# Performance work log

Measured on AMD Instinct MI355X. Metric: run time of the kernel, lower is better.

Reference implementation:

```python
import jax, jax.numpy as jnp
import numpy as np
import math

D_MODEL = 1024
N_HEADS = 16
D_K = D_MODEL // N_HEADS
B, S = 2, 2048


def setup_inputs() -> dict:
    key = jax.random.key(0)
    ks = jax.random.split(key, 11)
    sc = 1.0 / math.sqrt(D_MODEL)
    inp = {
        'q': jax.random.normal(ks[0], (B, S, D_MODEL), jnp.float32),
        'k': jax.random.normal(ks[1], (B, S, D_MODEL), jnp.float32),
        'v': jax.random.normal(ks[2], (B, S, D_MODEL), jnp.float32),
        'mask': jnp.tril(jnp.ones((S, S), jnp.int32))[None, None],  # [1,1,S,S] causal
        'W_q': jax.random.normal(ks[3], (D_MODEL, D_MODEL), jnp.float32) * sc,
        'b_q': jnp.zeros((D_MODEL,), jnp.float32),
        'W_k': jax.random.normal(ks[4], (D_MODEL, D_MODEL), jnp.float32) * sc,
        'b_k': jnp.zeros((D_MODEL,), jnp.float32),
        'W_v': jax.random.normal(ks[5], (D_MODEL, D_MODEL), jnp.float32) * sc,
        'b_v': jnp.zeros((D_MODEL,), jnp.float32),
        'W_o': jax.random.normal(ks[6], (D_MODEL, D_MODEL), jnp.float32) * sc,
        'b_o': jnp.zeros((D_MODEL,), jnp.float32),
    }
    return inp


def reference(q, k, v, mask, W_q, b_q, W_k, b_k, W_v, b_v, W_o, b_o):
    # Linear projections then split heads: [B,S,D] -> [B,H,S,d_k]
    def split_heads(x):
        b, s, _ = x.shape
        return x.reshape(b, s, N_HEADS, D_K).transpose(0, 2, 1, 3)

    Q = split_heads(q @ W_q + b_q)
    K = split_heads(k @ W_k + b_k)
    V = split_heads(v @ W_v + b_v)

    scores = jnp.einsum('bhqd,bhkd->bhqk', Q, K) / math.sqrt(D_K)
    scores = jnp.where(mask == 0, jnp.float32(-1e9), scores)
    attn = jax.nn.softmax(scores, axis=-1)  # dropout is identity in eval mode
    out = jnp.einsum('bhqk,bhkd->bhqd', attn, V)
    out = out.transpose(0, 2, 1, 3).reshape(q.shape[0], -1, D_MODEL)
    return out @ W_o + b_o
```

## Files before the change

kernel.cpp:

```cpp
#include <hip/hip_runtime.h>
#include <hip/hip_bf16.h>

#define D_MODEL 1024
#define S_LEN   2048
#define BATCH   2
#define NH      16
#define DK      64

typedef __bf16 bf16_t;
typedef __attribute__((ext_vector_type(8))) __bf16 bf16x8;
typedef __attribute__((ext_vector_type(4))) float f32x4;

#if __has_builtin(__builtin_amdgcn_exp2f)
#define EXP2F(x) __builtin_amdgcn_exp2f(x)
#else
#define EXP2F(x) exp2f(x)
#endif

#define Q_SCALE 0.1803368801111204f

#define GLDS16(gp, lp) __builtin_amdgcn_global_load_lds( \
    (const __attribute__((address_space(1))) void*)(gp), \
    (__attribute__((address_space(3))) void*)(lp), 16, 0, 0)

__global__ __launch_bounds__(256) void prep(
    const float* __restrict__ q, const float* __restrict__ k, const float* __restrict__ v,
    const float* __restrict__ Wq, const float* __restrict__ Wk,
    const float* __restrict__ Wv, const float* __restrict__ Wo,
    bf16_t* __restrict__ qkvb, bf16_t* __restrict__ WqkvT, bf16_t* __restrict__ WoT)
{
    __shared__ float t[32][33];
    const int tid = threadIdx.x;
    if (blockIdx.z < 3) {
        const long NELEM = (long)BATCH * S_LEN * D_MODEL;
        const float* src = (blockIdx.z == 0) ? q : (blockIdx.z == 1) ? k : v;
        long i = ((long)blockIdx.x * 256 + tid) * 8;
        float4 a = *(const float4*)(src + i);
        float4 b = *(const float4*)(src + i + 4);
        bf16x8 o;
        o[0] = (bf16_t)a.x; o[1] = (bf16_t)a.y; o[2] = (bf16_t)a.z; o[3] = (bf16_t)a.w;
        o[4] = (bf16_t)b.x; o[5] = (bf16_t)b.y; o[6] = (bf16_t)b.z; o[7] = (bf16_t)b.w;
        *(bf16x8*)(qkvb + blockIdx.z * NELEM + i) = o;
    } else {
        int wz = (blockIdx.z - 3) * 2048 + blockIdx.x;
        int mat = wz >> 10;
        int tile = wz & 1023;
        int bx = tile & 31, by = tile >> 5;
        const float* in = (mat == 0) ? Wq : (mat == 1) ? Wk : (mat == 2) ? Wv : Wo;
        bf16_t* out = (mat < 3) ? (WqkvT + (long)mat * D_MODEL * D_MODEL) : WoT;
        int tx = tid & 31, ty = tid >> 5;
        int gx = bx * 32, gy = by * 32;
#pragma unroll
        for (int i = 0; i < 32; i += 8)
            t[ty + i][tx] = in[(gy + ty + i) * D_MODEL + gx + tx];
        __syncthreads();
#pragma unroll
        for (int i = 0; i < 32; i += 8)
            out[(gx + ty + i) * D_MODEL + gy + tx] = (bf16_t)t[tx][ty + i];
    }
}

#define BM 128
#define BN 128
#define BKT 64

__device__ __forceinline__ void swizzle_xy(int bx, int by, int& n0, int& m0) {
    int lin = by * 8 + bx;
    n0 = (lin >> 5) * BN;
    m0 = (lin & 31) * BM;
}

template <int ROWS>
__device__ __forceinline__ void stage_swz(const bf16_t* __restrict__ G, int row0,
                                          int k0, bf16_t* __restrict__ Ls, int tid) {
#pragma unroll
    for (int it = 0; it < ROWS / 32; ++it) {
        int g = it * 256 + tid;
        int row = g >> 3;
        int c = (g & 7) ^ (row & 7);
        GLDS16(&G[(long)(row0 + row) * D_MODEL + k0 + c * 8],
               &Ls[(it * 256 + (tid & ~63)) * 8]);
    }
}

__device__ __forceinline__ bf16x8 frag_swz(const bf16_t* __restrict__ Ls, int row, int cg) {
    return *(const bf16x8*)(&Ls[(row * 8 + (cg ^ (row & 7))) * 8]);
}

constexpr int QKV_SMEM = (BM * BKT + BN * BKT) > (128 * 136) ? (BM * BKT + BN * BKT)
                                                             : (128 * 136);
__global__ __launch_bounds__(256) void gemm_qkv(
    const bf16_t* __restrict__ qkvb, const bf16_t* __restrict__ WqkvT,
    const float* __restrict__ bq, const float* __restrict__ bk, const float* __restrict__ bv,
    bf16_t* __restrict__ Qw, bf16_t* __restrict__ Kw, bf16_t* __restrict__ Vt)
{
    __shared__ __align__(16) bf16_t smem[QKV_SMEM];
    bf16_t* As = smem;
    bf16_t* Bs = smem + BM * BKT;
    const int z = blockIdx.z;
    const bf16_t* A  = qkvb + (long)z * BATCH * S_LEN * D_MODEL;
    const bf16_t* BT = WqkvT + (long)z * D_MODEL * D_MODEL;
    const float* bias = (z == 0) ? bq : (z == 1) ? bk : bv;
    bf16_t* Cb = (z == 0) ? Qw : (z == 1) ? Kw : Vt;
    const float oscale = (z == 0) ? Q_SCALE : 1.0f;

    const int tid  = threadIdx.x;
    const int wave = tid >> 6, lane = tid & 63;
    const int lrow = lane & 15, kgrp = lane >> 4;
    const int wm = (wave >> 1) * 64, wn = (wave & 1) * 64;
    int m0, n0;
    swizzle_xy(blockIdx.x, blockIdx.y, n0, m0);

    f32x4 acc[4][4] = {};

    for (int k0 = 0; k0 < D_MODEL; k0 += BKT) {
        stage_swz<BM>(A, m0, k0, As, tid);
        stage_swz<BN>(BT, n0, k0, Bs, tid);
        __syncthreads();
#pragma unroll
        for (int kk = 0; kk < 2; ++kk) {
            bf16x8 af[4], bfr[4];
#pragma unroll
            for (int mi = 0; mi < 4; ++mi)
                af[mi] = frag_swz(As, wm + mi * 16 + lrow, kk * 4 + kgrp);
#pragma unroll
            for (int ni = 0; ni < 4; ++ni)
                bfr[ni] = frag_swz(Bs, wn + ni * 16 + lrow, kk * 4 + kgrp);
#pragma unroll
            for (int mi = 0; mi < 4; ++mi)
#pragma unroll
                for (int ni = 0; ni < 4; ++ni)
                    acc[mi][ni] = __builtin_amdgcn_mfma_f32_16x16x32_bf16(af[mi], bfr[ni], acc[mi][ni], 0, 0, 0);
        }
        __syncthreads();
    }

    if (z != 2) {
#pragma unroll
        for (int mi = 0; mi < 4; ++mi)
#pragma unroll
            for (int ni = 0; ni < 4; ++ni) {
                int col = n0 + wn + ni * 16 + lrow;
                float bvf = bias[col];
#pragma unroll
                for (int r = 0; r < 4; ++r) {
                    int row = m0 + wm + mi * 16 + kgrp * 4 + r;
                    float vv = (acc[mi][ni][r] + bvf) * oscale;
                    int b = row >> 11, s = row & (S_LEN - 1);
                    int h = col >> 6, d = col & (DK - 1);
                    Cb[(((long)(b * NH + h) * S_LEN + s) * DK) + d] = (bf16_t)vv;
                }
            }
    } else {
        bf16_t* Ct = smem;
#pragma unroll
        for (int mi = 0; mi < 4; ++mi)
#pragma unroll
            for (int ni = 0; ni < 4; ++ni) {
                int cl = wn + ni * 16 + lrow;
                float bvf = bias[n0 + cl];
#pragma unroll
                for (int r = 0; r < 4; ++r) {
                    int rl = wm + mi * 16 + kgrp * 4 + r;
                    Ct[cl * 136 + rl] = (bf16_t)(acc[mi][ni][r] + bvf);
                }
            }
        __syncthreads();
        const int b = m0 >> 11, sbase = m0 & (S_LEN - 1);
#pragma unroll
        for (int pass = 0; pass < 4; ++pass) {
            int dl = pass * 32 + (tid >> 3);
            int sc = (tid & 7) * 16;
            int colg = n0 + dl;
            int h = colg >> 6, d = colg & (DK - 1);
            bf16_t* dst = Cb + (((long)(b * NH + h) * DK + d) * S_LEN + sbase + sc);
            *(bf16x8*)(dst)     = *(const bf16x8*)&Ct[dl * 136 + sc];
            *(bf16x8*)(dst + 8) = *(const bf16x8*)&Ct[dl * 136 + sc + 8];
        }
    }
}

#define OM 64
__global__ __launch_bounds__(256) void gemm_out(
    const bf16_t* __restrict__ A, const bf16_t* __restrict__ BT,
    const float* __restrict__ bias, float* __restrict__ Cf)
{
    __shared__ __align__(16) bf16_t As[OM * BKT];
    __shared__ __align__(16) bf16_t Bs[BN * BKT];
    const int tid  = threadIdx.x;
    const int wave = tid >> 6, lane = tid & 63;
    const int lrow = lane & 15, kgrp = lane >> 4;
    const int wm = (wave >> 1) * 32, wn = (wave & 1) * 64;
    int lin = blockIdx.y * 8 + blockIdx.x;
    int m0 = (lin & 63) * OM;
    int n0 = (lin >> 6) * BN;

    f32x4 acc[2][4] = {};

    for (int k0 = 0; k0 < D_MODEL; k0 += BKT) {
        stage_swz<OM>(A, m0, k0, As, tid);
        stage_swz<BN>(BT, n0, k0, Bs, tid);
        __syncthreads();
#pragma unroll
        for (int kk = 0; kk < 2; ++kk) {
            bf16x8 af[2], bfr[4];
#pragma unroll
            for (int mi = 0; mi < 2; ++mi)
                af[mi] = frag_swz(As, wm + mi * 16 + lrow, kk * 4 + kgrp);
#pragma unroll
            for (int ni = 0; ni < 4; ++ni)
                bfr[ni] = frag_swz(Bs, wn + ni * 16 + lrow, kk * 4 + kgrp);
#pragma unroll
            for (int mi = 0; mi < 2; ++mi)
#pragma unroll
                for (int ni = 0; ni < 4; ++ni)
                    acc[mi][ni] = __builtin_amdgcn_mfma_f32_16x16x32_bf16(af[mi], bfr[ni], acc[mi][ni], 0, 0, 0);
        }
        __syncthreads();
    }

#pragma unroll
    for (int mi = 0; mi < 2; ++mi)
#pragma unroll
        for (int ni = 0; ni < 4; ++ni) {
            int col = n0 + wn + ni * 16 + lrow;
            float bvf = bias[col];
#pragma unroll
            for (int r = 0; r < 4; ++r) {
                int row = m0 + wm + mi * 16 + kgrp * 4 + r;
                Cf[(long)row * D_MODEL + col] = acc[mi][ni][r] + bvf;
            }
        }
}

__device__ __forceinline__ void attn_one_qtile(
    int qi, int bh, int wave, int lrow, int kgrp,
    int r0, int c0, int r1,
    const bf16_t* __restrict__ Qh, const bf16_t* __restrict__ Kh,
    const bf16_t* __restrict__ Vth, bf16_t* __restrict__ O,
    bf16_t* __restrict__ Ks, bf16_t* __restrict__ Vs, bf16_t* __restrict__ Pw)
{
    const int q0 = qi * 64;
    const int qrow = q0 + wave * 16;

    bf16x8 qf[2];
#pragma unroll
    for (int kk = 0; kk < 2; ++kk)
        qf[kk] = *(const bf16x8*)(&Qh[(qrow + lrow) * DK + kk * 32 + kgrp * 8]);

    f32x4 acc[4] = {};
    float lsum[4] = {0.f, 0.f, 0.f, 0.f};

    const int nt = qi + 1;

    uint4 kpre0 = *(const uint4*)(&Kh[(long)r0 * DK + c0]);
    uint4 kpre1 = *(const uint4*)(&Kh[(long)r1 * DK + c0]);
    uint4 vpre0 = *(const uint4*)(&Vth[(long)r0 * S_LEN + c0]);
    uint4 vpre1 = *(const uint4*)(&Vth[(long)r1 * S_LEN + c0]);

    for (int t = 0; t < nt; ++t) {
        __syncthreads();
        *(uint4*)(&Ks[r0 * 72 + c0]) = kpre0;
        *(uint4*)(&Ks[r1 * 72 + c0]) = kpre1;
        *(uint4*)(&Vs[r0 * 72 + c0]) = vpre0;
        *(uint4*)(&Vs[r1 * 72 + c0]) = vpre1;
        if (t + 1 < nt) {
            const int j0n = (t + 1) * 64;
            kpre0 = *(const uint4*)(&Kh[(long)(j0n + r0) * DK + c0]);
            kpre1 = *(const uint4*)(&Kh[(long)(j0n + r1) * DK + c0]);
            vpre0 = *(const uint4*)(&Vth[(long)r0 * S_LEN + j0n + c0]);
            vpre1 = *(const uint4*)(&Vth[(long)r1 * S_LEN + j0n + c0]);
        }
        __syncthreads();

        const int j0 = t * 64;

        f32x4 sc[4] = {};
#pragma unroll
        for (int kk = 0; kk < 2; ++kk)
#pragma unroll
            for (int ni = 0; ni < 4; ++ni) {
                bf16x8 kf = *(const bf16x8*)(&Ks[(ni * 16 + lrow) * 72 + kk * 32 + kgrp * 8]);
                sc[ni] = __builtin_amdgcn_mfma_f32_16x16x32_bf16(qf[kk], kf, sc[ni], 0, 0, 0);
            }

        const bool needmask = (j0 + 63 > qrow);
        if (needmask) {
#pragma unroll
            for (int r = 0; r < 4; ++r) {
                int row = qrow + kgrp * 4 + r;
#pragma unroll
                for (int ni = 0; ni < 4; ++ni) {
                    int colj = j0 + ni * 16 + lrow;
                    float pv = EXP2F(sc[ni][r]);
                    if (colj > row) pv = 0.f;
                    lsum[r] += pv;
                    Pw[(kgrp * 4 + r) * 72 + ni * 16 + lrow] = (bf16_t)pv;
                }
            }
        } else {
#pragma unroll
            for (int r = 0; r < 4; ++r)
#pragma unroll
                for (int ni = 0; ni < 4; ++ni) {
                    float pv = EXP2F(sc[ni][r]);
                    lsum[r] += pv;
                    Pw[(kgrp * 4 + r) * 72 + ni * 16 + lrow] = (bf16_t)pv;
                }
        }

#pragma unroll
        for (int kk = 0; kk < 2; ++kk) {
            bf16x8 pf = *(const bf16x8*)(&Pw[lrow * 72 + kk * 32 + kgrp * 8]);
#pragma unroll
            for (int di = 0; di < 4; ++di) {
                bf16x8 vf = *(const bf16x8*)(&Vs[(di * 16 + lrow) * 72 + kk * 32 + kgrp * 8]);
                acc[di] = __builtin_amdgcn_mfma_f32_16x16x32_bf16(pf, vf, acc[di], 0, 0, 0);
            }
        }
    }

#pragma unroll
    for (int r = 0; r < 4; ++r)
#pragma unroll
        for (int off = 1; off < 16; off <<= 1)
            lsum[r] += __shfl_xor(lsum[r], off);

    const int b = bh >> 4, h = bh & (NH - 1);
#pragma unroll
    for (int r = 0; r < 4; ++r) {
        int s = qrow + kgrp * 4 + r;
        float inv = 1.f / lsum[r];
#pragma unroll
        for (int di = 0; di < 4; ++di) {
            int d = di * 16 + lrow;
            O[((long)(b * S_LEN + s)) * D_MODEL + h * DK + d] = (bf16_t)(acc[di][r] * inv);
        }
    }
}

__global__ __launch_bounds__(256, 2) void attn_kernel(
    const bf16_t* __restrict__ Q, const bf16_t* __restrict__ K,
    const bf16_t* __restrict__ Vt, bf16_t* __restrict__ O)
{
    __shared__ __align__(16) bf16_t Ks[64 * 72];
    __shared__ __align__(16) bf16_t Vs[64 * 72];
    __shared__ __align__(16) bf16_t Ps[4][16 * 72];

    const int bh = blockIdx.y;
    const int p  = blockIdx.x;
    const int tid = threadIdx.x, wave = tid >> 6, lane = tid & 63;
    const int lrow = lane & 15, kgrp = lane >> 4;

    const bf16_t* Qh  = Q  + (long)bh * S_LEN * DK;
    const bf16_t* Kh  = K  + (long)bh * S_LEN * DK;
    const bf16_t* Vth = Vt + (long)bh * DK * S_LEN;

    const int f0 = tid * 8;
    const int r0 = f0 >> 6, c0 = f0 & 63;
    const int r1 = (f0 + 2048) >> 6;

    attn_one_qtile(31 - p, bh, wave, lrow, kgrp, r0, c0, r1,
                   Qh, Kh, Vth, O, Ks, Vs, Ps[wave]);
    attn_one_qtile(p, bh, wave, lrow, kgrp, r0, c0, r1,
                   Qh, Kh, Vth, O, Ks, Vs, Ps[wave]);
}

extern "C" void kernel_launch(void* const* d_in, const int* in_sizes, int n_in,
                              void* d_out, int out_size, void* d_ws, size_t ws_size,
                              hipStream_t stream) {
    const float* q  = (const float*)d_in[0];
    const float* k  = (const float*)d_in[1];
    const float* v  = (const float*)d_in[2];
    const float* Wq = (const float*)d_in[4];
    const float* bq = (const float*)d_in[5];
    const float* Wk = (const float*)d_in[6];
    const float* bk = (const float*)d_in[7];
    const float* Wv = (const float*)d_in[8];
    const float* bv = (const float*)d_in[9];
    const float* Wo = (const float*)d_in[10];
    const float* bo = (const float*)d_in[11];

    char* ws = (char*)d_ws;
    const size_t Mi = 1024 * 1024;
    bf16_t* WqkvT = (bf16_t*)(ws);
    bf16_t* WoT   = (bf16_t*)(ws + 6 * Mi);
    bf16_t* Qw    = (bf16_t*)(ws + 8 * Mi);
    bf16_t* Kw    = (bf16_t*)(ws + 16 * Mi);
    bf16_t* Vtw   = (bf16_t*)(ws + 24 * Mi);
    bf16_t* qkvb  = (bf16_t*)(ws + 32 * Mi);
    bf16_t* Aw    = (bf16_t*)(ws + 32 * Mi);

    prep<<<dim3(2048, 1, 5), 256, 0, stream>>>(q, k, v, Wq, Wk, Wv, Wo,
                                               qkvb, WqkvT, WoT);

    gemm_qkv<<<dim3(D_MODEL / BN, (BATCH * S_LEN) / BM, 3), 256, 0, stream>>>(
        qkvb, WqkvT, bq, bk, bv, Qw, Kw, Vtw);

    attn_kernel<<<dim3(16, BATCH * NH), 256, 0, stream>>>(Qw, Kw, Vtw, Aw);

    gemm_out<<<dim3(D_MODEL / BN, (BATCH * S_LEN) / OM), 256, 0, stream>>>(
        Aw, WoT, bo, (float*)d_out);
}
```

Before: 228.5 us.

## Keep P in registers by computing transposed scores with permuted K rows

Swaps the MFMA operands so the score tile comes out transposed, and permutes the K rows as they are stored into LDS so that each lane's score accumulators line up directly with the B-operand layout of the P·V MFMA. This removes the per-wave LDS round-trip for the probability tile (the Ps buffer, its stores and reloads) and collapses the row-sum to one scalar per lane with fewer shuffles. In exchange, the masking index math and the final normalisation become more intricate, and they depend on the permutation being exactly right.

```diff
diff --git a/kernel.cpp b/kernel.cpp
--- a/kernel.cpp
+++ b/kernel.cpp
@@ -233,15 +233,20 @@
         }
 }
 
+__device__ __forceinline__ int krow_perm(int r) {
+    return ((r >> 5) + 2 * ((r >> 2) & 1)) * 16 + ((r >> 3) & 3) * 4 + (r & 3);
+}
+
 __device__ __forceinline__ void attn_one_qtile(
     int qi, int bh, int wave, int lrow, int kgrp,
     int r0, int c0, int r1,
     const bf16_t* __restrict__ Qh, const bf16_t* __restrict__ Kh,
     const bf16_t* __restrict__ Vth, bf16_t* __restrict__ O,
-    bf16_t* __restrict__ Ks, bf16_t* __restrict__ Vs, bf16_t* __restrict__ Pw)
+    bf16_t* __restrict__ Ks, bf16_t* __restrict__ Vs)
 {
     const int q0 = qi * 64;
     const int qrow = q0 + wave * 16;
+    const int qg = qrow + lrow;
 
     bf16x8 qf[2];
 #pragma unroll
@@ -249,9 +254,10 @@
         qf[kk] = *(const bf16x8*)(&Qh[(qrow + lrow) * DK + kk * 32 + kgrp * 8]);
 
     f32x4 acc[4] = {};
-    float lsum[4] = {0.f, 0.f, 0.f, 0.f};
+    float lsum = 0.f;
 
     const int nt = qi + 1;
+    const int rr0 = krow_perm(r0), rr1 = krow_perm(r1);
 
     uint4 kpre0 = *(const uint4*)(&Kh[(long)r0 * DK + c0]);
     uint4 kpre1 = *(const uint4*)(&Kh[(long)r1 * DK + c0]);
@@ -260,8 +266,8 @@
 
     for (int t = 0; t < nt; ++t) {
         __syncthreads();
-        *(uint4*)(&Ks[r0 * 72 + c0]) = kpre0;
-        *(uint4*)(&Ks[r1 * 72 + c0]) = kpre1;
+        *(uint4*)(&Ks[rr0 * 72 + c0]) = kpre0;
+        *(uint4*)(&Ks[rr1 * 72 + c0]) = kpre1;
         *(uint4*)(&Vs[r0 * 72 + c0]) = vpre0;
         *(uint4*)(&Vs[r1 * 72 + c0]) = vpre1;
         if (t + 1 < nt) {
@@ -281,56 +287,63 @@
 #pragma unroll
             for (int ni = 0; ni < 4; ++ni) {
                 bf16x8 kf = *(const bf16x8*)(&Ks[(ni * 16 + lrow) * 72 + kk * 32 + kgrp * 8]);
-                sc[ni] = __builtin_amdgcn_mfma_f32_16x16x32_bf16(qf[kk], kf, sc[ni], 0, 0, 0);
+                sc[ni] = __builtin_amdgcn_mfma_f32_16x16x32_bf16(kf, qf[kk], sc[ni], 0, 0, 0);
             }
 
+        float pb[4][4];
         const bool needmask = (j0 + 63 > qrow);
         if (needmask) {
 #pragma unroll
-            for (int r = 0; r < 4; ++r) {
-                int row = qrow + kgrp * 4 + r;
-#pragma unroll
-                for (int ni = 0; ni < 4; ++ni) {
-                    int colj = j0 + ni * 16 + lrow;
+            for (int ni = 0; ni < 4; ++ni) {
+                const int cb = j0 + (ni & 1) * 32 + kgrp * 8 + ((ni >> 1) << 2);
+#pragma unroll
+                for (int r = 0; r < 4; ++r) {
                     float pv = EXP2F(sc[ni][r]);
-                    if (colj > row) pv = 0.f;
-                    lsum[r] += pv;
-                    Pw[(kgrp * 4 + r) * 72 + ni * 16 + lrow] = (bf16_t)pv;
+                    if (cb + r > qg) pv = 0.f;
+                    lsum += pv;
+                    pb[ni][r] = pv;
                 }
             }
         } else {
 #pragma unroll
-            for (int r = 0; r < 4; ++r)
-#pragma unroll
-                for (int ni = 0; ni < 4; ++ni) {
+            for (int ni = 0; ni < 4; ++ni)
+#pragma unroll
+                for (int r = 0; r < 4; ++r) {
                     float pv = EXP2F(sc[ni][r]);
-                    lsum[r] += pv;
-                    Pw[(kgrp * 4 + r) * 72 + ni * 16 + lrow] = (bf16_t)pv;
+                    lsum += pv;
+                    pb[ni][r] = pv;
                 }
         }
 
-#pragma unroll
-        for (int kk = 0; kk < 2; ++kk) {
-            bf16x8 pf = *(const bf16x8*)(&Pw[lrow * 72 + kk * 32 + kgrp * 8]);
-#pragma unroll
-            for (int di = 0; di < 4; ++di) {
-                bf16x8 vf = *(const bf16x8*)(&Vs[(di * 16 + lrow) * 72 + kk * 32 + kgrp * 8]);
-                acc[di] = __builtin_amdgcn_mfma_f32_16x16x32_bf16(pf, vf, acc[di], 0, 0, 0);
-            }
-        }
-    }
-
-#pragma unroll
-    for (int r = 0; r < 4; ++r)
-#pragma unroll
-        for (int off = 1; off < 16; off <<= 1)
-            lsum[r] += __shfl_xor(lsum[r], off);
+        bf16x8 pf0, pf1;
+#pragma unroll
+        for (int r = 0; r < 4; ++r) {
+            pf0[r]     = (bf16_t)pb[0][r];
+            pf0[r + 4] = (bf16_t)pb[2][r];
+            pf1[r]     = (bf16_t)pb[1][r];
+            pf1[r + 4] = (bf16_t)pb[3][r];
+        }
+
+#pragma unroll
+        for (int di = 0; di < 4; ++di) {
+            bf16x8 vf = *(const bf16x8*)(&Vs[(di * 16 + lrow) * 72 + kgrp * 8]);
+            acc[di] = __builtin_amdgcn_mfma_f32_16x16x32_bf16(pf0, vf, acc[di], 0, 0, 0);
+        }
+#pragma unroll
+        for (int di = 0; di < 4; ++di) {
+            bf16x8 vf = *(const bf16x8*)(&Vs[(di * 16 + lrow) * 72 + 32 + kgrp * 8]);
+            acc[di] = __builtin_amdgcn_mfma_f32_16x16x32_bf16(pf1, vf, acc[di], 0, 0, 0);
+        }
+    }
+
+    lsum += __shfl_xor(lsum, 16);
+    lsum += __shfl_xor(lsum, 32);
 
     const int b = bh >> 4, h = bh & (NH - 1);
 #pragma unroll
     for (int r = 0; r < 4; ++r) {
+        float inv = 1.f / __shfl(lsum, kgrp * 4 + r);
         int s = qrow + kgrp * 4 + r;
-        float inv = 1.f / lsum[r];
 #pragma unroll
         for (int di = 0; di < 4; ++di) {
             int d = di * 16 + lrow;
@@ -345,7 +358,6 @@
 {
     __shared__ __align__(16) bf16_t Ks[64 * 72];
     __shared__ __align__(16) bf16_t Vs[64 * 72];
-    __shared__ __align__(16) bf16_t Ps[4][16 * 72];
 
     const int bh = blockIdx.y;
     const int p  = blockIdx.x;
@@ -361,9 +373,9 @@
     const int r1 = (f0 + 2048) >> 6;
 
     attn_one_qtile(31 - p, bh, wave, lrow, kgrp, r0, c0, r1,
-                   Qh, Kh, Vth, O, Ks, Vs, Ps[wave]);
+                   Qh, Kh, Vth, O, Ks, Vs);
     attn_one_qtile(p, bh, wave, lrow, kgrp, r0, c0, r1,
-                   Qh, Kh, Vth, O, Ks, Vs, Ps[wave]);
+                   Qh, Kh, Vth, O, Ks, Vs);
 }
 
 extern "C" void kernel_launch(void* const* d_in, const int* in_sizes, int n_in,
```

Result: faster. 222.0 us (-2.8%).
